# Optimization experiments

Measured on AMD Instinct MI355X. Metric: run time of the kernel, lower is better.

Reference implementation:

```python
import jax, jax.numpy as jnp
import numpy as np

HID = 512
HEADS = 8
HD = HID // HEADS
PF = 2048
EPS = 1e-5


def _layer_norm(x, g, b):
    m = jnp.mean(x, axis=-1, keepdims=True)
    v = jnp.mean((x - m) ** 2, axis=-1, keepdims=True)
    return (x - m) * jax.lax.rsqrt(v + EPS) * g + b


def setup_inputs() -> dict:
    key = jax.random.key(0)
    ks = jax.random.split(key, 24)
    s = 0.02
    p = {}
    p["src"] = jax.random.normal(ks[0], (2, 512, HID), dtype=jnp.float32)
    p["src_mask"] = jnp.ones((2, 1, 1, 512), dtype=jnp.int32)
    # projection weights stored as (in, out); Linear math y = x @ W + b
    p["Wq"] = jax.random.normal(ks[1], (HID, HID), dtype=jnp.float32) * s
    p["bq"] = jnp.zeros((HID,), jnp.float32)
    p["Wk"] = jax.random.normal(ks[2], (HID, HID), dtype=jnp.float32) * s
    p["bk"] = jnp.zeros((HID,), jnp.float32)
    p["Wv"] = jax.random.normal(ks[3], (HID, HID), dtype=jnp.float32) * s
    p["bv"] = jnp.zeros((HID,), jnp.float32)
    p["Wo"] = jax.random.normal(ks[4], (HID, HID), dtype=jnp.float32) * s
    p["bo"] = jnp.zeros((HID,), jnp.float32)
    # additive-attention params (per-head_dim)
    p["Wa"] = jax.random.normal(ks[5], (HD, HD), dtype=jnp.float32) * s
    p["ba"] = jnp.zeros((HD,), jnp.float32)
    p["Ua"] = jax.random.normal(ks[6], (HD, HD), dtype=jnp.float32) * s
    p["ub"] = jnp.zeros((HD,), jnp.float32)
    p["Vw"] = jax.random.normal(ks[7], (HD,), dtype=jnp.float32) * s
    p["Vb"] = jnp.zeros((), jnp.float32)
    # layer norms
    p["ln1_g"] = jnp.ones((HID,), jnp.float32)
    p["ln1_b"] = jnp.zeros((HID,), jnp.float32)
    p["ln2_g"] = jnp.ones((HID,), jnp.float32)
    p["ln2_b"] = jnp.zeros((HID,), jnp.float32)
    # FFN
    p["W1"] = jax.random.normal(ks[8], (HID, PF), dtype=jnp.float32) * s
    p["b1"] = jnp.zeros((PF,), jnp.float32)
    p["W2"] = jax.random.normal(ks[9], (PF, HID), dtype=jnp.float32) * s
    p["b2"] = jnp.zeros((HID,), jnp.float32)
    return p


def reference(src, src_mask, Wq, bq, Wk, bk, Wv, bv, Wo, bo,
              Wa, ba, Ua, ub, Vw, Vb, ln1_g, ln1_b, ln2_g, ln2_b,
              W1, b1, W2, b2):
    B, L, D = src.shape
    # project and split heads: (B, H, L, hd)
    def heads(x):
        return x.reshape(B, L, HEADS, HD).transpose(0, 2, 1, 3)
    Q = heads(src @ Wq + bq)
    K = heads(src @ Wk + bk)
    V = heads(src @ Wv + bv)
    Qa = Q @ Wa + ba          # (B,H,L,hd)
    Ka = K @ Ua + ub          # (B,H,L,hd)
    # additive (Bahdanau) scores: tanh broadcast to (B,H,Lq,Lk,hd), reduce with Vw
    t = jnp.tanh(Qa[:, :, :, None, :] + Ka[:, :, None, :, :])
    energy = jnp.einsum('bhqkd,d->bhqk', t, Vw) + Vb
    energy = jnp.where(src_mask == 0, jnp.float32(-1e10), energy)
    attention = jax.nn.softmax(energy, axis=-1)
    x = jnp.einsum('bhqk,bhkd->bhqd', attention, V)
    x = x.transpose(0, 2, 1, 3).reshape(B, L, D)
    attn_out = x @ Wo + bo
    src1 = _layer_norm(src + attn_out, ln1_g, ln1_b)
    ffn = jax.nn.relu(src1 @ W1 + b1) @ W2 + b2
    return _layer_norm(src1 + ffn, ln2_g, ln2_b)
```

## Files before the change

kernel.cpp:

```cpp
#include <hip/hip_runtime.h>

#define HID 512
#define HEADS 8
#define HD 64
#define PF 2048
#define LEN 512
#define EPS 1e-5f
#define LOG2E 1.44269504f

typedef __bf16 bf16x8 __attribute__((ext_vector_type(8)));
typedef float  f32x4  __attribute__((ext_vector_type(4)));

#define TC0 0.99990220f
#define TC1 (-0.33032631f)
#define TC2 0.11820859f
#define TC3 (-0.02619031f)
#define G3C1  (-0.99097893f)
#define G5C2  (0.59104295f)
#define G7C3  (-0.18333217f)
#define G10C2 (1.18208590f)
#define G21C3 (-0.54999651f)
#define G35C3 (-0.91666085f)

__device__ __forceinline__ void fuse_body(
    const float* __restrict__ Wbig, const float* __restrict__ Wsm,
    const float* __restrict__ bbig, const float* __restrict__ bsm,
    __bf16* __restrict__ outT, float* __restrict__ bout,
    int cchunk, int h, int t, float* smem) {
    float* wb_s = smem;
    float* wsm_s = smem + 4096;
    const int c0 = cchunk * 64;
    const int col = t & 63, rq = t >> 6;
    #pragma unroll
    for (int i = 0; i < 16; ++i) {
        int r = rq * 16 + i;
        wb_s[r * 64 + col]  = Wbig[(size_t)(c0 + r) * HID + h * 64 + col];
        wsm_s[r * 64 + col] = Wsm[r * 64 + col];
    }
    __syncthreads();
    float acc[16] = {};
    for (int d = 0; d < 64; ++d) {
        float wl = wsm_s[d * 64 + col];
        #pragma unroll
        for (int i = 0; i < 16; ++i)
            acc[i] += wb_s[(rq * 16 + i) * 64 + d] * wl;
    }
    #pragma unroll
    for (int i = 0; i < 16; ++i)
        outT[(size_t)(h * 64 + col) * HID + c0 + rq * 16 + i] = (__bf16)acc[i];
    if (cchunk == 0 && t < 64) {
        float bacc = bsm[col];
        for (int d = 0; d < 64; ++d)
            bacc += bbig[h * 64 + d] * wsm_s[d * 64 + col];
        bout[h * 64 + col] = bacc;
    }
}

__device__ __forceinline__ void cast_t_body(
    const float* __restrict__ W, __bf16* __restrict__ WT,
    int K, int N, int n0, int k0, int t, float* smem) {
    float* tile = smem;
    const int tx = t & 31, ty = t >> 5;
    #pragma unroll
    for (int i = 0; i < 4; ++i)
        tile[(ty + 8 * i) * 33 + tx] = W[(size_t)(k0 + ty + 8 * i) * N + n0 + tx];
    __syncthreads();
    #pragma unroll
    for (int i = 0; i < 4; ++i)
        WT[(size_t)(n0 + ty + 8 * i) * K + k0 + tx] = (__bf16)tile[tx * 33 + ty + 8 * i];
}

__global__ __launch_bounds__(256) void prep_all(
    const float* __restrict__ Wq, const float* __restrict__ Wa,
    const float* __restrict__ bq, const float* __restrict__ ba,
    const float* __restrict__ Wk, const float* __restrict__ Ua,
    const float* __restrict__ bk, const float* __restrict__ ub,
    const float* __restrict__ Wv, const float* __restrict__ bv,
    const float* __restrict__ Wo, const float* __restrict__ W1,
    const float* __restrict__ W2, const float* __restrict__ src,
    __bf16* __restrict__ WqkvT, float* __restrict__ bqkv,
    __bf16* __restrict__ WoT, __bf16* __restrict__ W1T,
    __bf16* __restrict__ W2T, __bf16* __restrict__ src_bf) {
    __shared__ float smem[8192];
    const int bid = blockIdx.x;
    const int t = threadIdx.x;
    if (bid < 64) {
        fuse_body(Wq, Wa, bq, ba, WqkvT, bqkv, bid & 7, bid >> 3, t, smem);
    } else if (bid < 128) {
        int q = bid - 64;
        fuse_body(Wk, Ua, bk, ub, WqkvT + (size_t)512 * HID, bqkv + 512, q & 7, q >> 3, t, smem);
    } else if (bid < 384) {
        int q = bid - 128;
        cast_t_body(Wv, WqkvT + (size_t)1024 * HID, HID, HID, (q & 15) * 32, (q >> 4) * 32, t, smem);
    } else if (bid < 640) {
        int q = bid - 384;
        cast_t_body(Wo, WoT, HID, HID, (q & 15) * 32, (q >> 4) * 32, t, smem);
    } else if (bid < 1664) {
        int q = bid - 640;
        cast_t_body(W1, W1T, HID, PF, (q & 63) * 32, (q >> 6) * 32, t, smem);
    } else if (bid < 2688) {
        int q = bid - 1664;
        cast_t_body(W2, W2T, PF, HID, (q & 15) * 32, (q >> 4) * 32, t, smem);
    } else if (bid < 2690) {
        int q = bid - 2688;
        bqkv[1024 + q * 256 + t] = bv[q * 256 + t];
    } else {
        int q = bid - 2690;
        int i = q * 256 + t;
        src_bf[i] = (__bf16)src[i];
    }
}

template <bool RELU, bool OUT_BF16, int KS>
__global__ __launch_bounds__(64) void gemm_mfma(
    const __bf16* __restrict__ A, const __bf16* __restrict__ BT,
    const float* __restrict__ bias, float* __restrict__ Cf,
    __bf16* __restrict__ Cb, int M, int N, int K) {
    const int m0 = blockIdx.x * 64;
    const int n0 = blockIdx.y * 64;
    const int ks = (KS > 1) ? blockIdx.z : 0;
    const int Kc = K / KS;
    const int l = threadIdx.x;
    const int r16 = l & 15;
    const int kof = (l >> 4) * 8 + ks * Kc;

    f32x4 acc[4][4] = {};
    const __bf16* Ap = A + (size_t)(m0 + r16) * K + kof;
    const __bf16* Bp = BT + (size_t)(n0 + r16) * K + kof;

    #pragma unroll 2
    for (int k0 = 0; k0 < Kc; k0 += 32) {
        bf16x8 a[4], b[4];
        #pragma unroll
        for (int mr = 0; mr < 4; ++mr)
            a[mr] = *(const bf16x8*)(Ap + (size_t)mr * 16 * K + k0);
        #pragma unroll
        for (int nr = 0; nr < 4; ++nr)
            b[nr] = *(const bf16x8*)(Bp + (size_t)nr * 16 * K + k0);
        #pragma unroll
        for (int mr = 0; mr < 4; ++mr)
            #pragma unroll
            for (int nr = 0; nr < 4; ++nr)
                acc[mr][nr] = __builtin_amdgcn_mfma_f32_16x16x32_bf16(a[mr], b[nr], acc[mr][nr], 0, 0, 0);
    }

    const int crow = (l >> 4) * 4;
    const int ccol = l & 15;
    float* Co = Cf + (size_t)ks * M * N;
    #pragma unroll
    for (int mr = 0; mr < 4; ++mr) {
        #pragma unroll
        for (int nr = 0; nr < 4; ++nr) {
            int n = n0 + nr * 16 + ccol;
            float bs = (ks == 0) ? bias[n] : 0.f;
            #pragma unroll
            for (int r = 0; r < 4; ++r) {
                int m = m0 + mr * 16 + crow + r;
                float v = acc[mr][nr][r] + bs;
                if (RELU) v = fmaxf(v, 0.f);
                if (OUT_BF16) Cb[(size_t)m * N + n] = (__bf16)v;
                else          Co[(size_t)m * N + n] = v;
            }
        }
    }
}

__global__ __launch_bounds__(64) void qkv_feat(
    const __bf16* __restrict__ A, const __bf16* __restrict__ BT,
    const float* __restrict__ bqkv, const float* __restrict__ Vw,
    __bf16* __restrict__ Af, __bf16* __restrict__ Bf,
    __bf16* __restrict__ VT) {
    __shared__ float tile[64][65];
    const int m0 = blockIdx.x * 64;
    const int by = blockIdx.y;
    const int n0 = by * 64;
    const int type = by >> 3;
    const int h = by & 7;
    const int b = m0 >> 9;
    const int bh = b * 8 + h;
    const int l0 = m0 & 511;
    const int l = threadIdx.x;
    const int r16 = l & 15;
    const int g = l >> 4;
    const int kof = g * 8;

    f32x4 acc[4][4] = {};
    const __bf16* Ap = A + (size_t)(m0 + r16) * HID + kof;
    const __bf16* Bp = BT + (size_t)(n0 + r16) * HID + kof;
    #pragma unroll 2
    for (int k0 = 0; k0 < HID; k0 += 32) {
        bf16x8 a[4], bb[4];
        #pragma unroll
        for (int mr = 0; mr < 4; ++mr)
            a[mr] = *(const bf16x8*)(Ap + (size_t)mr * 16 * HID + k0);
        #pragma unroll
        for (int nr = 0; nr < 4; ++nr)
            bb[nr] = *(const bf16x8*)(Bp + (size_t)nr * 16 * HID + k0);
        #pragma unroll
        for (int mr = 0; mr < 4; ++mr)
            #pragma unroll
            for (int nr = 0; nr < 4; ++nr)
                acc[mr][nr] = __builtin_amdgcn_mfma_f32_16x16x32_bf16(a[mr], bb[nr], acc[mr][nr], 0, 0, 0);
    }

    const int crow = g * 4;
    const int ccol = r16;
    if (type == 0) {
        #pragma unroll
        for (int nr = 0; nr < 4; ++nr) {
            int d = nr * 16 + ccol;
            float bs = bqkv[n0 + d];
            #pragma unroll
            for (int mr = 0; mr < 4; ++mr)
                #pragma unroll
                for (int r = 0; r < 4; ++r) {
                    int lrow = l0 + mr * 16 + crow + r;
                    float x = acc[mr][nr][r] + bs;
                    float x2 = x * x, x3 = x2 * x, x4 = x2 * x2, x6 = x4 * x2;
                    bf16x8 f;
                    f[0] = (__bf16)1.0f; f[1] = (__bf16)x;
                    f[2] = (__bf16)x2;   f[3] = (__bf16)x3;
                    f[4] = (__bf16)x4;   f[5] = (__bf16)(x4 * x);
                    f[6] = (__bf16)x6;   f[7] = (__bf16)(x6 * x);
                    *(bf16x8*)(Af + ((size_t)(bh * LEN + lrow)) * 512 + d * 8) = f;
                }
        }
    } else if (type == 1) {
        #pragma unroll
        for (int nr = 0; nr < 4; ++nr) {
            int d = nr * 16 + ccol;
            float bs = bqkv[n0 + d];
            float w = Vw[d];
            #pragma unroll
            for (int mr = 0; mr < 4; ++mr)
                #pragma unroll
                for (int r = 0; r < 4; ++r) {
                    int lrow = l0 + mr * 16 + crow + r;
                    float y = acc[mr][nr][r] + bs;
                    float y2 = y * y;
                    bf16x8 f;
                    f[0] = (__bf16)(w * (y * (((TC3 * y2 + TC2) * y2 + TC1) * y2 + TC0)));
                    f[1] = (__bf16)(w * (((G7C3 * y2 + G5C2) * y2 + G3C1) * y2 + TC0));
                    f[2] = (__bf16)(w * (y * ((G21C3 * y2 + G10C2) * y2 + G3C1)));
                    f[3] = (__bf16)(w * ((G35C3 * y2 + G10C2) * y2 + TC1));
                    f[4] = (__bf16)(w * (y * (G35C3 * y2 + G5C2)));
                    f[5] = (__bf16)(w * (G21C3 * y2 + TC2));
                    f[6] = (__bf16)(w * (G7C3 * y));
                    f[7] = (__bf16)(w * TC3);
                    *(bf16x8*)(Bf + ((size_t)(bh * LEN + lrow)) * 512 + d * 8) = f;
                }
        }
    } else {
        #pragma unroll
        for (int nr = 0; nr < 4; ++nr) {
            int d = nr * 16 + ccol;
            float bs = bqkv[n0 + d];
            #pragma unroll
            for (int mr = 0; mr < 4; ++mr)
                #pragma unroll
                for (int r = 0; r < 4; ++r)
                    tile[mr * 16 + crow + r][d] = acc[mr][nr][r] + bs;
        }
        __syncthreads();
        for (int dd = 0; dd < 64; ++dd)
            VT[((size_t)(bh * 64 + dd)) * LEN + l0 + l] = (__bf16)tile[l][dd];
    }
}

__global__ __launch_bounds__(256) void energy_sm(
    const __bf16* __restrict__ Af, const __bf16* __restrict__ Bf,
    const int* __restrict__ mask, __bf16* __restrict__ P) {
    __shared__ float rs[32][5];
    const int bid = blockIdx.x;
    const int wgid = (bid & 7) * 32 + (bid >> 3);
    const int bh = wgid >> 4;
    const int m0 = (wgid & 15) * 32;
    const int b = bh >> 3;
    const int w = threadIdx.x >> 6;
    const int l = threadIdx.x & 63;
    const int r16 = l & 15, g = l >> 4, kof = g * 8;
    const int c0 = w * 128;

    const __bf16* Ap = Af + ((size_t)(bh * LEN + m0 + r16)) * 512 + kof;
    const __bf16* Bp = Bf + ((size_t)(bh * LEN + c0 + r16)) * 512 + kof;

    f32x4 acc[2][8] = {};
    #pragma unroll 2
    for (int k0 = 0; k0 < 512; k0 += 32) {
        bf16x8 a0 = *(const bf16x8*)(Ap + k0);
        bf16x8 a1 = *(const bf16x8*)(Ap + 16 * 512 + k0);
        #pragma unroll
        for (int nr = 0; nr < 8; ++nr) {
            bf16x8 bb = *(const bf16x8*)(Bp + (size_t)nr * 16 * 512 + k0);
            acc[0][nr] = __builtin_amdgcn_mfma_f32_16x16x32_bf16(a0, bb, acc[0][nr], 0, 0, 0);
            acc[1][nr] = __builtin_amdgcn_mfma_f32_16x16x32_bf16(a1, bb, acc[1][nr], 0, 0, 0);
        }
    }

    float rsum[2][4] = {};
    #pragma unroll
    for (int nr = 0; nr < 8; ++nr) {
        int col = c0 + nr * 16 + r16;
        float mk = (mask[b * LEN + col] == 0) ? 0.f : 1.f;
        #pragma unroll
        for (int mr = 0; mr < 2; ++mr)
            #pragma unroll
            for (int r = 0; r < 4; ++r) {
                float pv = __builtin_amdgcn_exp2f(acc[mr][nr][r] * LOG2E) * mk;
                acc[mr][nr][r] = pv;
                rsum[mr][r] += pv;
            }
    }
    #pragma unroll
    for (int off = 1; off <= 8; off <<= 1)
        #pragma unroll
        for (int mr = 0; mr < 2; ++mr)
            #pragma unroll
            for (int r = 0; r < 4; ++r)
                rsum[mr][r] += __shfl_xor(rsum[mr][r], off);
    if (r16 == 0) {
        #pragma unroll
        for (int mr = 0; mr < 2; ++mr)
            #pragma unroll
            for (int r = 0; r < 4; ++r)
                rs[mr * 16 + g * 4 + r][w] = rsum[mr][r];
    }
    __syncthreads();
    float inv_[2][4];
    #pragma unroll
    for (int mr = 0; mr < 2; ++mr)
        #pragma unroll
        for (int r = 0; r < 4; ++r) {
            int row = mr * 16 + g * 4 + r;
            float tot = rs[row][0] + rs[row][1] + rs[row][2] + rs[row][3];
            inv_[mr][r] = __builtin_amdgcn_rcpf(tot);
        }
    #pragma unroll
    for (int mr = 0; mr < 2; ++mr)
        #pragma unroll
        for (int nr = 0; nr < 8; ++nr) {
            int col = c0 + nr * 16 + r16;
            #pragma unroll
            for (int r = 0; r < 4; ++r) {
                int row = m0 + mr * 16 + g * 4 + r;
                P[((size_t)(bh * LEN + row)) * LEN + col] = (__bf16)(acc[mr][nr][r] * inv_[mr][r]);
            }
        }
}

__global__ __launch_bounds__(64) void pv_gemm(
    const __bf16* __restrict__ P, const __bf16* __restrict__ VT,
    __bf16* __restrict__ X) {
    const int bid = blockIdx.x;
    const int wgid = (bid & 7) * 32 + (bid >> 3);
    const int bh = wgid >> 4, b = bh >> 3, h = bh & 7;
    const int m0 = (wgid & 15) * 32;
    const int l = threadIdx.x;
    const int r16 = l & 15;
    const int kof = (l >> 4) * 8;

    const __bf16* Ap = P + ((size_t)(bh * LEN + m0 + r16)) * LEN + kof;
    const __bf16* Bp = VT + ((size_t)(bh * 64 + r16)) * LEN + kof;

    f32x4 acc[2][4] = {};
    #pragma unroll 2
    for (int k0 = 0; k0 < 512; k0 += 32) {
        bf16x8 a0 = *(const bf16x8*)(Ap + k0);
        bf16x8 a1 = *(const bf16x8*)(Ap + 16 * LEN + k0);
        #pragma unroll
        for (int nr = 0; nr < 4; ++nr) {
            bf16x8 bb = *(const bf16x8*)(Bp + (size_t)nr * 16 * LEN + k0);
            acc[0][nr] = __builtin_amdgcn_mfma_f32_16x16x32_bf16(a0, bb, acc[0][nr], 0, 0, 0);
            acc[1][nr] = __builtin_amdgcn_mfma_f32_16x16x32_bf16(a1, bb, acc[1][nr], 0, 0, 0);
        }
    }

    const int crow = (l >> 4) * 4;
    const int ccol = l & 15;
    #pragma unroll
    for (int mr = 0; mr < 2; ++mr)
        #pragma unroll
        for (int nr = 0; nr < 4; ++nr)
            #pragma unroll
            for (int r = 0; r < 4; ++r) {
                int q = m0 + mr * 16 + crow + r;
                int dd = nr * 16 + ccol;
                X[(size_t)(b * LEN + q) * HID + h * 64 + dd] = (__bf16)acc[mr][nr][r];
            }
}

template <bool WB, int NS>
__global__ __launch_bounds__(256) void ln_kernel(
    const float* __restrict__ A, const float* __restrict__ Bsrc,
    const float* __restrict__ g, const float* __restrict__ beta,
    float* __restrict__ out, __bf16* __restrict__ outb) {
    const int row = blockIdx.x;
    const int t = threadIdx.x;
    float x0 = Bsrc[(size_t)row * HID + t];
    float x1 = Bsrc[(size_t)row * HID + t + 256];
    #pragma unroll
    for (int s = 0; s < NS; ++s) {
        x0 += A[(size_t)s * 524288 + (size_t)row * HID + t];
        x1 += A[(size_t)s * 524288 + (size_t)row * HID + t + 256];
    }
    float s0 = x0 + x1, ss = x0 * x0 + x1 * x1;
    #pragma unroll
    for (int off = 32; off; off >>= 1) {
        s0 += __shfl_xor(s0, off);
        ss += __shfl_xor(ss, off);
    }
    __shared__ float rsm[4], rss[4];
    const int lane = t & 63, wv = t >> 6;
    if (lane == 0) { rsm[wv] = s0; rss[wv] = ss; }
    __syncthreads();
    s0 = rsm[0] + rsm[1] + rsm[2] + rsm[3];
    ss = rss[0] + rss[1] + rss[2] + rss[3];
    float mean = s0 * (1.0f / HID);
    float var = ss * (1.0f / HID) - mean * mean;
    float inv = rsqrtf(var + EPS);
    float y0 = (x0 - mean) * inv * g[t] + beta[t];
    float y1 = (x1 - mean) * inv * g[t + 256] + beta[t + 256];
    out[(size_t)row * HID + t] = y0;
    out[(size_t)row * HID + t + 256] = y1;
    if (WB) {
        outb[(size_t)row * HID + t] = (__bf16)y0;
        outb[(size_t)row * HID + t + 256] = (__bf16)y1;
    }
}


extern "C" void kernel_launch(void* const* d_in, const int* in_sizes, int n_in,
                              void* d_out, int out_size, void* d_ws, size_t ws_size,
                              hipStream_t stream) {
    const float* src   = (const float*)d_in[0];
    const int*   mask  = (const int*)d_in[1];
    const float* Wq    = (const float*)d_in[2];
    const float* bq    = (const float*)d_in[3];
    const float* Wk    = (const float*)d_in[4];
    const float* bk    = (const float*)d_in[5];
    const float* Wv    = (const float*)d_in[6];
    const float* bv    = (const float*)d_in[7];
    const float* Wo    = (const float*)d_in[8];
    const float* bo    = (const float*)d_in[9];
    const float* Wa    = (const float*)d_in[10];
    const float* ba    = (const float*)d_in[11];
    const float* Ua    = (const float*)d_in[12];
    const float* ub    = (const float*)d_in[13];
    const float* Vw    = (const float*)d_in[14];
    const float* ln1g  = (const float*)d_in[16];
    const float* ln1b  = (const float*)d_in[17];
    const float* ln2g  = (const float*)d_in[18];
    const float* ln2b  = (const float*)d_in[19];
    const float* W1    = (const float*)d_in[20];
    const float* b1    = (const float*)d_in[21];
    const float* W2    = (const float*)d_in[22];
    const float* b2    = (const float*)d_in[23];
    float* out = (float*)d_out;

    float* ws = (float*)d_ws;
    size_t off = 0;
    auto alloc = [&](size_t nf) { float* p = ws + off; off += nf; return p; };

    __bf16* WqkvT  = (__bf16*)alloc(393216);
    __bf16* WoT    = (__bf16*)alloc(131072);
    __bf16* W1T    = (__bf16*)alloc(524288);
    __bf16* W2T    = (__bf16*)alloc(524288);
    float*  bqkv   = alloc(1536);
    __bf16* src_bf = (__bf16*)alloc(262144);
    __bf16* Af     = (__bf16*)alloc(2097152);
    __bf16* Bf     = (__bf16*)alloc(2097152);
    __bf16* VT     = (__bf16*)alloc(262144);
    __bf16* P      = (__bf16*)alloc(2097152);
    __bf16* x_bf   = (__bf16*)alloc(262144);
    float*  tmp    = alloc(2097152);
    float*  src1   = alloc(524288);
    __bf16* s1_bf  = (__bf16*)alloc(262144);
    __bf16* h1     = (__bf16*)alloc(1048576);

    const int M = 2 * LEN;

    prep_all<<<4738, 256, 0, stream>>>(Wq, Wa, bq, ba, Wk, Ua, bk, ub,
                                       Wv, bv, Wo, W1, W2, src,
                                       WqkvT, bqkv, WoT, W1T, W2T, src_bf);

    qkv_feat<<<dim3(16, 24), 64, 0, stream>>>(src_bf, WqkvT, bqkv, Vw, Af, Bf, VT);

    energy_sm<<<256, 256, 0, stream>>>(Af, Bf, mask, P);

    pv_gemm<<<256, 64, 0, stream>>>(P, VT, x_bf);

    gemm_mfma<false, false, 2><<<dim3(16, 8, 2), 64, 0, stream>>>(
        x_bf, WoT, bo, tmp, nullptr, M, HID, HID);

    ln_kernel<true, 2><<<M, 256, 0, stream>>>(tmp, src, ln1g, ln1b, src1, s1_bf);

    gemm_mfma<true, true, 1><<<dim3(16, 32), 64, 0, stream>>>(
        s1_bf, W1T, b1, nullptr, h1, M, PF, HID);

    gemm_mfma<false, false, 4><<<dim3(16, 8, 4), 64, 0, stream>>>(
        h1, W2T, b2, tmp, nullptr, M, HID, PF);

    ln_kernel<false, 4><<<M, 256, 0, stream>>>(tmp, src1, ln2g, ln2b, out, nullptr);
}
```

Baseline: 107.0 us.

## Fuse softmax-probability and PV GEMM into one attention kernel via LDS

Merges the energy/softmax kernel and the P·V GEMM into a single kernel. Normalized probabilities are written to a swizzled 32KB LDS tile instead of a global P buffer, then four waves each compute a row-half/k-half partial of P·V and reduce the partials through shared memory. This removes one launch and the global round trip of the probability matrix. It also raises the k-loop unroll factor from 2 to 4 in the GEMM kernels, which costs extra LDS and registers and may lower occupancy.

After: 102.2 us. 4.5% less time.

```diff
diff --git a/kernel.cpp b/kernel.cpp
--- a/kernel.cpp
+++ b/kernel.cpp
@@ -128,7 +128,7 @@
     const __bf16* Ap = A + (size_t)(m0 + r16) * K + kof;
     const __bf16* Bp = BT + (size_t)(n0 + r16) * K + kof;
 
-    #pragma unroll 2
+    #pragma unroll 4
     for (int k0 = 0; k0 < Kc; k0 += 32) {
         bf16x8 a[4], b[4];
         #pragma unroll
@@ -187,7 +187,7 @@
     f32x4 acc[4][4] = {};
     const __bf16* Ap = A + (size_t)(m0 + r16) * HID + kof;
     const __bf16* Bp = BT + (size_t)(n0 + r16) * HID + kof;
-    #pragma unroll 2
+    #pragma unroll 4
     for (int k0 = 0; k0 < HID; k0 += 32) {
         bf16x8 a[4], bb[4];
         #pragma unroll
@@ -267,15 +267,18 @@
     }
 }
 
-__global__ __launch_bounds__(256) void energy_sm(
+__global__ __launch_bounds__(256) void attn_psum(
     const __bf16* __restrict__ Af, const __bf16* __restrict__ Bf,
-    const int* __restrict__ mask, __bf16* __restrict__ P) {
+    const __bf16* __restrict__ VT, const int* __restrict__ mask,
+    __bf16* __restrict__ X) {
+    __shared__ __align__(16) char pls[32 * 1024];
+    __shared__ float psum[4][16][64];
     __shared__ float rs[32][5];
     const int bid = blockIdx.x;
     const int wgid = (bid & 7) * 32 + (bid >> 3);
     const int bh = wgid >> 4;
     const int m0 = (wgid & 15) * 32;
-    const int b = bh >> 3;
+    const int b = bh >> 3, h = bh & 7;
     const int w = threadIdx.x >> 6;
     const int l = threadIdx.x & 63;
     const int r16 = l & 15, g = l >> 4, kof = g * 8;
@@ -285,7 +288,7 @@
     const __bf16* Bp = Bf + ((size_t)(bh * LEN + c0 + r16)) * 512 + kof;
 
     f32x4 acc[2][8] = {};
-    #pragma unroll 2
+    #pragma unroll 4
     for (int k0 = 0; k0 < 512; k0 += 32) {
         bf16x8 a0 = *(const bf16x8*)(Ap + k0);
         bf16x8 a1 = *(const bf16x8*)(Ap + 16 * 512 + k0);
@@ -342,51 +345,39 @@
             int col = c0 + nr * 16 + r16;
             #pragma unroll
             for (int r = 0; r < 4; ++r) {
-                int row = m0 + mr * 16 + g * 4 + r;
-                P[((size_t)(bh * LEN + row)) * LEN + col] = (__bf16)(acc[mr][nr][r] * inv_[mr][r]);
+                int row = mr * 16 + g * 4 + r;
+                int byte = (row * 1024 + col * 2) ^ ((row & 7) << 4);
+                *(__bf16*)(pls + byte) = (__bf16)(acc[mr][nr][r] * inv_[mr][r]);
             }
         }
-}
-
-__global__ __launch_bounds__(64) void pv_gemm(
-    const __bf16* __restrict__ P, const __bf16* __restrict__ VT,
-    __bf16* __restrict__ X) {
-    const int bid = blockIdx.x;
-    const int wgid = (bid & 7) * 32 + (bid >> 3);
-    const int bh = wgid >> 4, b = bh >> 3, h = bh & 7;
-    const int m0 = (wgid & 15) * 32;
-    const int l = threadIdx.x;
-    const int r16 = l & 15;
-    const int kof = (l >> 4) * 8;
-
-    const __bf16* Ap = P + ((size_t)(bh * LEN + m0 + r16)) * LEN + kof;
-    const __bf16* Bp = VT + ((size_t)(bh * 64 + r16)) * LEN + kof;
-
-    f32x4 acc[2][4] = {};
-    #pragma unroll 2
-    for (int k0 = 0; k0 < 512; k0 += 32) {
-        bf16x8 a0 = *(const bf16x8*)(Ap + k0);
-        bf16x8 a1 = *(const bf16x8*)(Ap + 16 * LEN + k0);
+    __syncthreads();
+
+    const int rh = w >> 1, kh = w & 1;
+    f32x4 oc[4] = {};
+    const __bf16* Vp = VT + ((size_t)(bh * 64 + r16)) * LEN + kh * 256 + kof;
+    #pragma unroll 4
+    for (int k0 = 0; k0 < 256; k0 += 32) {
+        int row = rh * 16 + r16;
+        int byte = (row * 1024 + (kh * 256 + k0 + kof) * 2) ^ ((row & 7) << 4);
+        bf16x8 pa = *(const bf16x8*)(pls + byte);
         #pragma unroll
         for (int nr = 0; nr < 4; ++nr) {
-            bf16x8 bb = *(const bf16x8*)(Bp + (size_t)nr * 16 * LEN + k0);
-            acc[0][nr] = __builtin_amdgcn_mfma_f32_16x16x32_bf16(a0, bb, acc[0][nr], 0, 0, 0);
-            acc[1][nr] = __builtin_amdgcn_mfma_f32_16x16x32_bf16(a1, bb, acc[1][nr], 0, 0, 0);
-        }
-    }
-
-    const int crow = (l >> 4) * 4;
-    const int ccol = l & 15;
-    #pragma unroll
-    for (int mr = 0; mr < 2; ++mr)
-        #pragma unroll
-        for (int nr = 0; nr < 4; ++nr)
-            #pragma unroll
-            for (int r = 0; r < 4; ++r) {
-                int q = m0 + mr * 16 + crow + r;
-                int dd = nr * 16 + ccol;
-                X[(size_t)(b * LEN + q) * HID + h * 64 + dd] = (__bf16)acc[mr][nr][r];
-            }
+            bf16x8 vb = *(const bf16x8*)(Vp + (size_t)nr * 16 * LEN + k0);
+            oc[nr] = __builtin_amdgcn_mfma_f32_16x16x32_bf16(pa, vb, oc[nr], 0, 0, 0);
+        }
+    }
+    #pragma unroll
+    for (int nr = 0; nr < 4; ++nr)
+        #pragma unroll
+        for (int r = 0; r < 4; ++r)
+            psum[w][g * 4 + r][nr * 16 + r16] = oc[nr][r];
+    __syncthreads();
+    for (int i = threadIdx.x; i < 32 * 64; i += 256) {
+        int row = i >> 6, d = i & 63;
+        int rh2 = row >> 4, rr = row & 15;
+        float v = psum[rh2 * 2][rr][d] + psum[rh2 * 2 + 1][rr][d];
+        X[(size_t)(b * LEN + m0 + row) * HID + h * 64 + d] = (__bf16)v;
+    }
 }
 
 template <bool WB, int NS>
@@ -470,7 +461,6 @@
     __bf16* Af     = (__bf16*)alloc(2097152);
     __bf16* Bf     = (__bf16*)alloc(2097152);
     __bf16* VT     = (__bf16*)alloc(262144);
-    __bf16* P      = (__bf16*)alloc(2097152);
     __bf16* x_bf   = (__bf16*)alloc(262144);
     float*  tmp    = alloc(2097152);
     float*  src1   = alloc(524288);
@@ -485,9 +475,7 @@
 
     qkv_feat<<<dim3(16, 24), 64, 0, stream>>>(src_bf, WqkvT, bqkv, Vw, Af, Bf, VT);
 
-    energy_sm<<<256, 256, 0, stream>>>(Af, Bf, mask, P);
-
-    pv_gemm<<<256, 64, 0, stream>>>(P, VT, x_bf);
+    attn_psum<<<256, 256, 0, stream>>>(Af, Bf, VT, mask, x_bf);
 
     gemm_mfma<false, false, 2><<<dim3(16, 8, 2), 64, 0, stream>>>(
         x_bf, WoT, bo, tmp, nullptr, M, HID, HID);
```
